# Optimization experiments

Hardware: AMD Instinct MI355X
Metric: run time of the kernel (lower is better)

The kernel has to match this reference:

```python
import jax, jax.numpy as jnp
import numpy as np

NUM_FREQS = 10  # get_embedder_nerf(10, input_dims=3) -> 3 + 3*2*10 = 63 dims


def nerf_embed(x):
    # x: [..., 3]; order per NeRF embedder: [x, sin(f0*x), cos(f0*x), sin(f1*x), ...]
    freqs = (2.0 ** jnp.arange(NUM_FREQS)).astype(x.dtype)           # [10]
    xb = x[..., None, :] * freqs[:, None]                            # [..., 10, 3]
    sc = jnp.stack([jnp.sin(xb), jnp.cos(xb)], axis=-2)              # [..., 10, 2, 3]
    return jnp.concatenate([x, sc.reshape(x.shape[:-1] + (60,))], axis=-1)


def setup_inputs() -> dict:
    key = jax.random.key(0)
    ks = jax.random.split(key, 16)
    B, H, W = 4, 256, 256
    V, F = 50000, 100000
    FEAT, SHAPE_FEAT, STYLE = 256, 128, 256
    D_IN = FEAT + SHAPE_FEAT + 63 + STYLE  # 703
    HID = 256
    s = 0.05
    return {
        "pix_to_face": jax.random.randint(ks[0], (B, H, W), 0, F),
        "bary_coords": jax.random.uniform(ks[1], (B, H, W, 3), dtype=jnp.float32),
        "faces": jax.random.randint(ks[2], (F, 3), 0, V),
        "feature": jax.random.normal(ks[3], (V, FEAT), dtype=jnp.float32),
        "shape_features": jax.random.normal(ks[4], (V, SHAPE_FEAT), dtype=jnp.float32),
        "color_bg": jax.random.uniform(ks[5], (B, 3, 1, 1), dtype=jnp.float32),
        "style_latent": jax.random.normal(ks[6], (1, STYLE), dtype=jnp.float32),
        "w1": jax.random.normal(ks[7], (D_IN, HID), dtype=jnp.float32) * s,
        "b1": jax.random.normal(ks[8], (HID,), dtype=jnp.float32) * s,
        "w2": jax.random.normal(ks[9], (HID, HID), dtype=jnp.float32) * s,
        "b2": jax.random.normal(ks[10], (HID,), dtype=jnp.float32) * s,
        "w3": jax.random.normal(ks[11], (HID, 3), dtype=jnp.float32) * s,
        "b3": jax.random.normal(ks[12], (3,), dtype=jnp.float32) * s,
    }


def reference(pix_to_face, bary_coords, faces, feature, shape_features,
              color_bg, style_latent, w1, b1, w2, b2, w3, b3):
    B, H, W = pix_to_face.shape
    mask = pix_to_face > 0                                           # foreground pixels
    vidx = faces[pix_to_face]                                        # [B,H,W,3] vertex ids
    # gather per-vertex features then barycentric-weighted mean over the 3 verts
    fv = feature[vidx]                                               # [B,H,W,3,256]
    ff = jnp.einsum('bhwvc,bhwv->bhwc', fv, bary_coords) / 3.0       # .mean(dim=3)
    sv = shape_features[vidx]                                        # [B,H,W,3,128]
    sf = jnp.einsum('bhwvc,bhwv->bhwc', sv, bary_coords) / 3.0
    emb = nerf_embed(bary_coords)                                    # [B,H,W,63]
    style = jnp.broadcast_to(style_latent[0], (B, H, W, style_latent.shape[-1]))
    x = jnp.concatenate([ff, sf, emb, style], axis=-1)               # [B,H,W,703]
    h = jax.nn.relu(x @ w1 + b1)
    h = jax.nn.relu(h @ w2 + b2)
    out = jax.nn.relu(h @ w3 + b3)                                   # mlp ends with ReLU
    colors = out - 1.0                                               # use_act=True, tanh=False
    bg = color_bg[:, :, 0, 0][:, None, None, :]                      # [B,1,1,3]
    buf = jnp.where(mask[..., None], colors, bg)                     # scatter to image
    return jnp.concatenate([buf, mask.astype(buf.dtype)[..., None]], axis=-1)  # [B,H,W,4]
```

## Files before the change

### kernel.cpp

```cpp
#include <hip/hip_runtime.h>
#include <math.h>


typedef _Float16 hv8 __attribute__((ext_vector_type(8)));
typedef __attribute__((ext_vector_type(4))) float f32x4;

#define TILE_M 64

__device__ inline int swzE(int row, int k) { return row * 64  + (k ^ ((row & 7) << 3)); }
__device__ inline int swzH(int row, int k) { return row * 256 + (k ^ ((row & 7) << 3)); }
__device__ inline int swzA(int row, int k) { return row * 384 + (k ^ ((row & 7) << 3)); }

__global__ __launch_bounds__(256)
void prep_weights(const float* __restrict__ style,
                  const float* __restrict__ w1, const float* __restrict__ b1,
                  const float* __restrict__ w2, const float* __restrict__ w3,
                  _Float16* __restrict__ w1T, _Float16* __restrict__ w2T,
                  _Float16* __restrict__ w3T, float* __restrict__ b1p)
{
    const int j = blockIdx.x;
    const int t = threadIdx.x;
    if (j < 256) {
        float part = style[t] * w1[(size_t)(447 + t) * 256 + j];
        #pragma unroll
        for (int off = 32; off; off >>= 1) part += __shfl_down(part, off, 64);
        __shared__ float red[4];
        if ((t & 63) == 0) red[t >> 6] = part;
        __syncthreads();
        if (t == 0) b1p[j] = b1[j] + red[0] + red[1] + red[2] + red[3];
        for (int k = t; k < 448; k += 256) {
            float v = (k < 447) ? w1[(size_t)k * 256 + j] : 0.0f;
            if (k < 384) v *= (1.0f / 3.0f);
            w1T[(size_t)j * 448 + k] = (_Float16)v;
        }
    } else if (j < 512) {
        const int jj = j - 256;
        w2T[(size_t)jj * 256 + t] = (_Float16)w2[(size_t)t * 256 + jj];
    } else {
        #pragma unroll
        for (int r = 0; r < 16; ++r)
            w3T[r * 256 + t] = (r < 3) ? (_Float16)w3[t * 3 + r] : (_Float16)0.0f;
    }
}

__global__ __launch_bounds__(256, 2)
void pgemm(const float* __restrict__ feat, const float* __restrict__ shp,
           const _Float16* __restrict__ w1T, _Float16* __restrict__ P, int nV)
{
    __shared__ _Float16 as[64 * 384];
    const int tid = threadIdx.x;
    const int n0 = blockIdx.x * 64;
    const int lane = tid & 63, wv = tid >> 6;
    const int nbase = wv << 6, l15 = lane & 15, kq = lane >> 4;

    const hv8* bp[4];
    #pragma unroll
    for (int nf = 0; nf < 4; ++nf)
        bp[nf] = (const hv8*)(w1T + (size_t)(nbase + nf * 16 + l15) * 448 + (kq << 3));
    hv8 bv[3][4];
    auto loadB = [&](int t, hv8* dst) {
        #pragma unroll
        for (int nf = 0; nf < 4; ++nf) dst[nf] = bp[nf][t << 2];
    };
    loadB(0, bv[0]); loadB(1, bv[1]); loadB(2, bv[2]);

    #pragma unroll
    for (int i = 0; i < 12; ++i) {
        const int id = tid + i * 256;
        const int row = id / 48;
        const int g = id - row * 48;
        int v = n0 + row; if (v >= nV) v = nV - 1;
        const float* s = (g < 32) ? (feat + (size_t)v * 256 + g * 8)
                                  : (shp  + (size_t)v * 128 + (g - 32) * 8);
        const float4 a = ((const float4*)s)[0];
        const float4 b = ((const float4*)s)[1];
        hv8 h = { (_Float16)a.x, (_Float16)a.y, (_Float16)a.z, (_Float16)a.w,
                  (_Float16)b.x, (_Float16)b.y, (_Float16)b.z, (_Float16)b.w };
        *(hv8*)(&as[swzA(row, g * 8)]) = h;
    }
    f32x4 acc[4][4];
    #pragma unroll
    for (int mf = 0; mf < 4; ++mf)
        #pragma unroll
        for (int nf = 0; nf < 4; ++nf) acc[mf][nf] = (f32x4){0.f, 0.f, 0.f, 0.f};
    __syncthreads();

    auto loadA = [&](int t, hv8* dst) {
        #pragma unroll
        for (int mf = 0; mf < 4; ++mf)
            dst[mf] = *(const hv8*)(as + swzA(mf * 16 + l15, (t << 5) | (kq << 3)));
    };
    hv8 av[2][4];
    loadA(0, av[0]);
    #pragma unroll
    for (int t = 0; t < 12; ++t) {
        if (t + 1 < 12) loadA(t + 1, av[(t + 1) & 1]);
        const hv8* avt = av[t & 1];
        const hv8* bvt = bv[t % 3];
        __builtin_amdgcn_s_setprio(1);
        #pragma unroll
        for (int mf = 0; mf < 4; ++mf)
            #pragma unroll
            for (int nf = 0; nf < 4; ++nf)
                acc[mf][nf] = __builtin_amdgcn_mfma_f32_16x16x32_f16(avt[mf], bvt[nf], acc[mf][nf], 0, 0, 0);
        __builtin_amdgcn_s_setprio(0);
        if (t + 3 < 12) loadB(t + 3, bv[t % 3]);
    }
    #pragma unroll
    for (int mf = 0; mf < 4; ++mf)
        #pragma unroll
        for (int nf = 0; nf < 4; ++nf) {
            const int col = nbase + nf * 16 + l15;
            const int r0 = mf * 16 + (kq << 2);
            #pragma unroll
            for (int r = 0; r < 4; ++r) {
                const int v = n0 + r0 + r;
                if (v < nV) P[(size_t)v * 256 + col] = (_Float16)acc[mf][nf][r];
            }
        }
}

__global__ __launch_bounds__(256, 3)
void renderer(const int* __restrict__ pix, const float* __restrict__ bary,
              const int* __restrict__ faces,
              const _Float16* __restrict__ P,
              const float* __restrict__ color_bg,
              const float* __restrict__ b2g,
              const float* __restrict__ b3,
              const _Float16* __restrict__ w1T,
              const _Float16* __restrict__ w2T,
              const _Float16* __restrict__ w3T,
              const float* __restrict__ b1p,
              float* __restrict__ out)
{
    __shared__ _Float16 embs[64 * 64];
    __shared__ _Float16 pb[64 * 256];
    __shared__ int   vidx[TILE_M][3];
    __shared__ float bcs[TILE_M][3];

    const int tid = threadIdx.x;
    const int cpx = gridDim.x >> 3;
    const int bid = (blockIdx.x & 7) * cpx + (blockIdx.x >> 3);
    const int n0  = bid * TILE_M;

    const int lane  = tid & 63;
    const int wv    = tid >> 6;
    const int nbase = wv << 6;
    const int l15   = lane & 15;
    const int kq    = lane >> 4;

    if (tid < TILE_M) {
        const int n = n0 + tid;
        const int face = pix[n];
        vidx[tid][0] = faces[face * 3 + 0];
        vidx[tid][1] = faces[face * 3 + 1];
        vidx[tid][2] = faces[face * 3 + 2];
        bcs[tid][0] = bary[n * 3 + 0];
        bcs[tid][1] = bary[n * 3 + 1];
        bcs[tid][2] = bary[n * 3 + 2];
    }
    __syncthreads();

    const int gp = tid >> 5;
    const int c8 = (tid & 31) << 3;

    hv8 g0[3], g1[3];
    auto loadG = [&](hv8* g, const int b) {
        const int p = b * 8 + gp;
        g[0] = *(const hv8*)(P + (size_t)vidx[p][0] * 256 + c8);
        g[1] = *(const hv8*)(P + (size_t)vidx[p][1] * 256 + c8);
        g[2] = *(const hv8*)(P + (size_t)vidx[p][2] * 256 + c8);
    };
    auto blendG = [&](hv8* g, const int b) {
        const int p = b * 8 + gp;
        const _Float16 c0 = (_Float16)bcs[p][0];
        const _Float16 c1 = (_Float16)bcs[p][1];
        const _Float16 c2 = (_Float16)bcs[p][2];
        *(hv8*)(&pb[swzH(p, c8)]) = g[0] * c0 + g[1] * c1 + g[2] * c2;
    };

    loadG(g0, 0);
    loadG(g1, 1);

    {
        const int p = tid >> 2;
        const int e16 = (tid & 3) << 4;
        const float c0 = bcs[p][0], c1 = bcs[p][1], c2 = bcs[p][2];
        #pragma unroll
        for (int hh = 0; hh < 2; ++hh) {
            hv8 h;
            #pragma unroll
            for (int i = 0; i < 8; ++i) {
                const int s = e16 + hh * 8 + i;
                float v;
                if (s < 3) v = (s == 0) ? c0 : ((s == 1) ? c1 : c2);
                else if (s < 63) {
                    const int q = s - 3;
                    const int f = q / 6;
                    const int rem = q - f * 6;
                    const int d = (rem >= 3) ? rem - 3 : rem;
                    const float bd = (d == 0) ? c0 : ((d == 1) ? c1 : c2);
                    const float arg = bd * (float)(1 << f);
                    v = (rem < 3) ? __sinf(arg) : __cosf(arg);
                } else v = 0.0f;
                h[i] = (_Float16)v;
            }
            *(hv8*)(&embs[swzE(p, e16 + hh * 8)]) = h;
        }
    }

    blendG(g0, 0); loadG(g0, 2);
    blendG(g1, 1); loadG(g1, 3);
    blendG(g0, 2); loadG(g0, 4);
    blendG(g1, 3); loadG(g1, 5);
    blendG(g0, 4); loadG(g0, 6);
    blendG(g1, 5); loadG(g1, 7);
    blendG(g0, 6);
    blendG(g1, 7);

    f32x4 acc[4][4];
    #pragma unroll
    for (int nf = 0; nf < 4; ++nf) {
        const float b = b1p[nbase + nf * 16 + l15];
        #pragma unroll
        for (int mf = 0; mf < 4; ++mf) acc[mf][nf] = (f32x4){b, b, b, b};
    }
    __syncthreads();

    #pragma unroll
    for (int t = 0; t < 2; ++t) {
        hv8 ave[4], bve[4];
        #pragma unroll
        for (int nf = 0; nf < 4; ++nf)
            bve[nf] = *(const hv8*)(w1T + (size_t)(nbase + nf * 16 + l15) * 448 + 384 + (t << 5) + (kq << 3));
        #pragma unroll
        for (int mf = 0; mf < 4; ++mf)
            ave[mf] = *(const hv8*)(embs + swzE(mf * 16 + l15, (t << 5) | (kq << 3)));
        __builtin_amdgcn_s_setprio(1);
        #pragma unroll
        for (int mf = 0; mf < 4; ++mf)
            #pragma unroll
            for (int nf = 0; nf < 4; ++nf)
                acc[mf][nf] = __builtin_amdgcn_mfma_f32_16x16x32_f16(ave[mf], bve[nf], acc[mf][nf], 0, 0, 0);
        __builtin_amdgcn_s_setprio(0);
    }

    #pragma unroll
    for (int mf = 0; mf < 4; ++mf)
        #pragma unroll
        for (int nf = 0; nf < 4; ++nf) {
            const int col = nbase + nf * 16 + l15;
            const int r0 = mf * 16 + (kq << 2);
            #pragma unroll
            for (int r = 0; r < 4; ++r) {
                const int sl = swzH(r0 + r, col);
                const float pv = (float)pb[sl];
                pb[sl] = (_Float16)fmaxf(acc[mf][nf][r] + pv, 0.0f);
            }
            const float b = b2g[col];
            acc[mf][nf] = (f32x4){b, b, b, b};
        }
    __syncthreads();

    const hv8* bp2[4];
    #pragma unroll
    for (int nf = 0; nf < 4; ++nf)
        bp2[nf] = (const hv8*)(w2T + (size_t)(nbase + nf * 16 + l15) * 256 + (kq << 3));
    #pragma unroll
    for (int t = 0; t < 8; ++t) {
        hv8 av[4], bv[4];
        #pragma unroll
        for (int nf = 0; nf < 4; ++nf) bv[nf] = bp2[nf][t << 2];
        #pragma unroll
        for (int mf = 0; mf < 4; ++mf)
            av[mf] = *(const hv8*)(pb + swzH(mf * 16 + l15, (t << 5) | (kq << 3)));
        __builtin_amdgcn_s_setprio(1);
        #pragma unroll
        for (int mf = 0; mf < 4; ++mf)
            #pragma unroll
            for (int nf = 0; nf < 4; ++nf)
                acc[mf][nf] = __builtin_amdgcn_mfma_f32_16x16x32_f16(av[mf], bv[nf], acc[mf][nf], 0, 0, 0);
        __builtin_amdgcn_s_setprio(0);
    }

    __syncthreads();
    #pragma unroll
    for (int mf = 0; mf < 4; ++mf)
        #pragma unroll
        for (int nf = 0; nf < 4; ++nf) {
            const int col = nbase + nf * 16 + l15;
            const int r0 = mf * 16 + (kq << 2);
            #pragma unroll
            for (int r = 0; r < 4; ++r)
                pb[swzH(r0 + r, col)] = (_Float16)fmaxf(acc[mf][nf][r], 0.0f);
        }

    hv8 bw3[8];
    #pragma unroll
    for (int t = 0; t < 8; ++t)
        bw3[t] = *(const hv8*)(w3T + l15 * 256 + ((t << 5) | (kq << 3)));
    __syncthreads();

    f32x4 acc3 = (f32x4){0.f, 0.f, 0.f, 0.f};
    #pragma unroll
    for (int t = 0; t < 8; ++t) {
        const hv8 av3 = *(const hv8*)(pb + swzH((wv << 4) + l15, (t << 5) | (kq << 3)));
        acc3 = __builtin_amdgcn_mfma_f32_16x16x32_f16(av3, bw3[t], acc3, 0, 0, 0);
    }
    if (l15 < 4) {
        const int ch = l15;
        #pragma unroll
        for (int r = 0; r < 4; ++r) {
            const int p = (wv << 4) + (kq << 2) + r;
            const int n = n0 + p;
            const bool m = pix[n] > 0;
            float v;
            if (ch == 3) v = m ? 1.0f : 0.0f;
            else         v = m ? (fmaxf(acc3[r] + b3[ch], 0.0f) - 1.0f)
                               : color_bg[(n >> 16) * 3 + ch];
            out[(size_t)n * 4 + ch] = v;
        }
    }
}

extern "C" void kernel_launch(void* const* d_in, const int* in_sizes, int n_in,
                              void* d_out, int out_size, void* d_ws, size_t ws_size,
                              hipStream_t stream) {
    const int*   pix      = (const int*)  d_in[0];
    const float* bary     = (const float*)d_in[1];
    const int*   faces    = (const int*)  d_in[2];
    const float* feature  = (const float*)d_in[3];
    const float* shapef   = (const float*)d_in[4];
    const float* color_bg = (const float*)d_in[5];
    const float* style    = (const float*)d_in[6];
    const float* w1       = (const float*)d_in[7];
    const float* b1       = (const float*)d_in[8];
    const float* w2       = (const float*)d_in[9];
    const float* b2       = (const float*)d_in[10];
    const float* w3       = (const float*)d_in[11];
    const float* b3       = (const float*)d_in[12];
    float* out = (float*)d_out;

    const int nV = in_sizes[3] / 256;

    char* ws = (char*)d_ws;
    _Float16* w1T  = (_Float16*)ws;
    _Float16* w2T  = (_Float16*)(ws + 229376);
    float*    b1p  = (float*)   (ws + 360448);
    _Float16* w3T  = (_Float16*)(ws + 361472);
    _Float16* Ptab = (_Float16*)(ws + 369664);

    hipLaunchKernelGGL(prep_weights, dim3(513), dim3(256), 0, stream,
                       style, w1, b1, w2, w3, w1T, w2T, w3T, b1p);
    hipLaunchKernelGGL(pgemm, dim3((nV + 63) / 64), dim3(256), 0, stream,
                       feature, shapef, w1T, Ptab, nV);

    const int npix = in_sizes[0];
    hipLaunchKernelGGL(renderer, dim3(npix / TILE_M), dim3(256), 0, stream,
                       pix, bary, faces, Ptab, color_bg,
                       b2, b3, w1T, w2T, w3T, b1p, out);
}
```

Baseline: 185.7 us.

## Make each wave own 16 pixel rows end to end and drop block barriers

The renderer now gives each wave its own 16-pixel slice and private shared buffer, running gather, blend, all three MLP layers and output without __syncthreads, using only lgkmcnt waits. The embedding fragment is built directly in registers, and the b1 bias is folded into the blended gathered features. Shared memory per block shrinks and launch bounds rise to 4 blocks per SM to raise occupancy. In exchange, each wave now reads all of w1/w2 from global/L1 per 16 rows instead of sharing a 64-row tile, so weight traffic per pixel grows roughly fourfold, and b1 is now added in fp16 rather than fp32.

```diff
diff --git a/kernel.cpp b/kernel.cpp
--- a/kernel.cpp
+++ b/kernel.cpp
@@ -7,8 +7,7 @@
 
 #define TILE_M 64
 
-__device__ inline int swzE(int row, int k) { return row * 64  + (k ^ ((row & 7) << 3)); }
-__device__ inline int swzH(int row, int k) { return row * 256 + (k ^ ((row & 7) << 3)); }
+__device__ inline int swzW(int row, int k) { return row * 256 + (k ^ ((row & 7) << 3)); }
 __device__ inline int swzA(int row, int k) { return row * 384 + (k ^ ((row & 7) << 3)); }
 
 __global__ __launch_bounds__(256)
@@ -120,78 +119,70 @@
         }
 }
 
-__global__ __launch_bounds__(256, 3)
+__global__ __launch_bounds__(256, 4)
 void renderer(const int* __restrict__ pix, const float* __restrict__ bary,
               const int* __restrict__ faces,
               const _Float16* __restrict__ P,
               const float* __restrict__ color_bg,
               const float* __restrict__ b2g,
-              const float* __restrict__ b3,
+              const float* __restrict__ b3g,
               const _Float16* __restrict__ w1T,
               const _Float16* __restrict__ w2T,
               const _Float16* __restrict__ w3T,
               const float* __restrict__ b1p,
               float* __restrict__ out)
 {
-    __shared__ _Float16 embs[64 * 64];
-    __shared__ _Float16 pb[64 * 256];
-    __shared__ int   vidx[TILE_M][3];
-    __shared__ float bcs[TILE_M][3];
-
-    const int tid = threadIdx.x;
-    const int cpx = gridDim.x >> 3;
-    const int bid = (blockIdx.x & 7) * cpx + (blockIdx.x >> 3);
-    const int n0  = bid * TILE_M;
-
-    const int lane  = tid & 63;
-    const int wv    = tid >> 6;
-    const int nbase = wv << 6;
-    const int l15   = lane & 15;
-    const int kq    = lane >> 4;
-
-    if (tid < TILE_M) {
-        const int n = n0 + tid;
+    __shared__ _Float16 pbAll[4][16 * 256];
+    __shared__ int   vidx[4][16][3];
+    __shared__ float bcs[4][16][3];
+
+    const int tid  = threadIdx.x;
+    const int lane = tid & 63;
+    const int wv   = tid >> 6;
+    const int cpx  = gridDim.x >> 3;
+    const int bid  = (blockIdx.x & 7) * cpx + (blockIdx.x >> 3);
+    const int n0   = bid * TILE_M + wv * 16;
+    const int l15  = lane & 15;
+    const int kq   = lane >> 4;
+    _Float16* pbw = &pbAll[wv][0];
+
+    if (lane < 16) {
+        const int n = n0 + lane;
         const int face = pix[n];
-        vidx[tid][0] = faces[face * 3 + 0];
-        vidx[tid][1] = faces[face * 3 + 1];
-        vidx[tid][2] = faces[face * 3 + 2];
-        bcs[tid][0] = bary[n * 3 + 0];
-        bcs[tid][1] = bary[n * 3 + 1];
-        bcs[tid][2] = bary[n * 3 + 2];
-    }
-    __syncthreads();
-
-    const int gp = tid >> 5;
-    const int c8 = (tid & 31) << 3;
-
+        vidx[wv][lane][0] = faces[face * 3 + 0];
+        vidx[wv][lane][1] = faces[face * 3 + 1];
+        vidx[wv][lane][2] = faces[face * 3 + 2];
+        bcs[wv][lane][0] = bary[n * 3 + 0];
+        bcs[wv][lane][1] = bary[n * 3 + 1];
+        bcs[wv][lane][2] = bary[n * 3 + 2];
+    }
+    asm volatile("s_waitcnt lgkmcnt(0)" ::: "memory");
+
+    const int gp = lane >> 5;
+    const int c8 = (lane & 31) << 3;
     hv8 g0[3], g1[3];
-    auto loadG = [&](hv8* g, const int b) {
-        const int p = b * 8 + gp;
-        g[0] = *(const hv8*)(P + (size_t)vidx[p][0] * 256 + c8);
-        g[1] = *(const hv8*)(P + (size_t)vidx[p][1] * 256 + c8);
-        g[2] = *(const hv8*)(P + (size_t)vidx[p][2] * 256 + c8);
+    auto loadG = [&](hv8* g, int b) {
+        const int p = (b << 1) + gp;
+        g[0] = *(const hv8*)(P + (size_t)vidx[wv][p][0] * 256 + c8);
+        g[1] = *(const hv8*)(P + (size_t)vidx[wv][p][1] * 256 + c8);
+        g[2] = *(const hv8*)(P + (size_t)vidx[wv][p][2] * 256 + c8);
     };
-    auto blendG = [&](hv8* g, const int b) {
-        const int p = b * 8 + gp;
-        const _Float16 c0 = (_Float16)bcs[p][0];
-        const _Float16 c1 = (_Float16)bcs[p][1];
-        const _Float16 c2 = (_Float16)bcs[p][2];
-        *(hv8*)(&pb[swzH(p, c8)]) = g[0] * c0 + g[1] * c1 + g[2] * c2;
-    };
-
     loadG(g0, 0);
     loadG(g1, 1);
 
+    const float4 bb0 = *(const float4*)(b1p + c8);
+    const float4 bb1 = *(const float4*)(b1p + c8 + 4);
+    const hv8 b1h = { (_Float16)bb0.x, (_Float16)bb0.y, (_Float16)bb0.z, (_Float16)bb0.w,
+                      (_Float16)bb1.x, (_Float16)bb1.y, (_Float16)bb1.z, (_Float16)bb1.w };
+
+    hv8 ave[2];
     {
-        const int p = tid >> 2;
-        const int e16 = (tid & 3) << 4;
-        const float c0 = bcs[p][0], c1 = bcs[p][1], c2 = bcs[p][2];
-        #pragma unroll
-        for (int hh = 0; hh < 2; ++hh) {
-            hv8 h;
+        const float c0 = bcs[wv][l15][0], c1 = bcs[wv][l15][1], c2 = bcs[wv][l15][2];
+        #pragma unroll
+        for (int t = 0; t < 2; ++t) {
             #pragma unroll
             for (int i = 0; i < 8; ++i) {
-                const int s = e16 + hh * 8 + i;
+                const int s = (t << 5) + (kq << 3) + i;
                 float v;
                 if (s < 3) v = (s == 0) ? c0 : ((s == 1) ? c1 : c2);
                 else if (s < 63) {
@@ -203,12 +194,18 @@
                     const float arg = bd * (float)(1 << f);
                     v = (rem < 3) ? __sinf(arg) : __cosf(arg);
                 } else v = 0.0f;
-                h[i] = (_Float16)v;
+                ave[t][i] = (_Float16)v;
             }
-            *(hv8*)(&embs[swzE(p, e16 + hh * 8)]) = h;
-        }
-    }
-
+        }
+    }
+
+    auto blendG = [&](hv8* g, int b) {
+        const int p = (b << 1) + gp;
+        const _Float16 d0 = (_Float16)bcs[wv][p][0];
+        const _Float16 d1 = (_Float16)bcs[wv][p][1];
+        const _Float16 d2 = (_Float16)bcs[wv][p][2];
+        *(hv8*)(&pbw[swzW(p, c8)]) = g[0] * d0 + g[1] * d1 + g[2] * d2 + b1h;
+    };
     blendG(g0, 0); loadG(g0, 2);
     blendG(g1, 1); loadG(g1, 3);
     blendG(g0, 2); loadG(g0, 4);
@@ -217,106 +214,92 @@
     blendG(g1, 5); loadG(g1, 7);
     blendG(g0, 6);
     blendG(g1, 7);
-
-    f32x4 acc[4][4];
-    #pragma unroll
-    for (int nf = 0; nf < 4; ++nf) {
-        const float b = b1p[nbase + nf * 16 + l15];
-        #pragma unroll
-        for (int mf = 0; mf < 4; ++mf) acc[mf][nf] = (f32x4){b, b, b, b};
-    }
-    __syncthreads();
-
-    #pragma unroll
-    for (int t = 0; t < 2; ++t) {
-        hv8 ave[4], bve[4];
-        #pragma unroll
-        for (int nf = 0; nf < 4; ++nf)
-            bve[nf] = *(const hv8*)(w1T + (size_t)(nbase + nf * 16 + l15) * 448 + 384 + (t << 5) + (kq << 3));
-        #pragma unroll
-        for (int mf = 0; mf < 4; ++mf)
-            ave[mf] = *(const hv8*)(embs + swzE(mf * 16 + l15, (t << 5) | (kq << 3)));
-        __builtin_amdgcn_s_setprio(1);
-        #pragma unroll
-        for (int mf = 0; mf < 4; ++mf)
-            #pragma unroll
-            for (int nf = 0; nf < 4; ++nf)
-                acc[mf][nf] = __builtin_amdgcn_mfma_f32_16x16x32_f16(ave[mf], bve[nf], acc[mf][nf], 0, 0, 0);
-        __builtin_amdgcn_s_setprio(0);
-    }
-
-    #pragma unroll
-    for (int mf = 0; mf < 4; ++mf)
-        #pragma unroll
-        for (int nf = 0; nf < 4; ++nf) {
-            const int col = nbase + nf * 16 + l15;
-            const int r0 = mf * 16 + (kq << 2);
-            #pragma unroll
-            for (int r = 0; r < 4; ++r) {
-                const int sl = swzH(r0 + r, col);
-                const float pv = (float)pb[sl];
-                pb[sl] = (_Float16)fmaxf(acc[mf][nf][r] + pv, 0.0f);
+    asm volatile("s_waitcnt lgkmcnt(0)" ::: "memory");
+
+    #pragma unroll
+    for (int h = 0; h < 2; ++h) {
+        const int cb = h << 7;
+        f32x4 acc[8];
+        #pragma unroll
+        for (int n = 0; n < 8; ++n) {
+            const int col = cb + n * 16 + l15;
+            const int r0 = kq << 2;
+            #pragma unroll
+            for (int r = 0; r < 4; ++r)
+                acc[n][r] = (float)pbw[swzW(r0 + r, col)];
+        }
+        #pragma unroll
+        for (int t = 0; t < 2; ++t) {
+            __builtin_amdgcn_s_setprio(1);
+            #pragma unroll
+            for (int n = 0; n < 8; ++n) {
+                const hv8 bve = *(const hv8*)(w1T + (size_t)(cb + n * 16 + l15) * 448 + 384 + (t << 5) + (kq << 3));
+                acc[n] = __builtin_amdgcn_mfma_f32_16x16x32_f16(ave[t], bve, acc[n], 0, 0, 0);
             }
-            const float b = b2g[col];
-            acc[mf][nf] = (f32x4){b, b, b, b};
-        }
-    __syncthreads();
-
-    const hv8* bp2[4];
-    #pragma unroll
-    for (int nf = 0; nf < 4; ++nf)
-        bp2[nf] = (const hv8*)(w2T + (size_t)(nbase + nf * 16 + l15) * 256 + (kq << 3));
+            __builtin_amdgcn_s_setprio(0);
+        }
+        #pragma unroll
+        for (int n = 0; n < 8; ++n) {
+            const int col = cb + n * 16 + l15;
+            const int r0 = kq << 2;
+            #pragma unroll
+            for (int r = 0; r < 4; ++r)
+                pbw[swzW(r0 + r, col)] = (_Float16)fmaxf(acc[n][r], 0.0f);
+        }
+    }
+    asm volatile("s_waitcnt lgkmcnt(0)" ::: "memory");
+
+    hv8 avh[8];
+    #pragma unroll
+    for (int t = 0; t < 8; ++t)
+        avh[t] = *(const hv8*)(pbw + swzW(l15, (t << 5) | (kq << 3)));
+    #pragma unroll
+    for (int h = 0; h < 2; ++h) {
+        const int cb = h << 7;
+        f32x4 acc[8];
+        #pragma unroll
+        for (int n = 0; n < 8; ++n) {
+            const float b = b2g[cb + n * 16 + l15];
+            acc[n] = (f32x4){b, b, b, b};
+        }
+        #pragma unroll
+        for (int t = 0; t < 8; ++t) {
+            __builtin_amdgcn_s_setprio(1);
+            #pragma unroll
+            for (int n = 0; n < 8; ++n) {
+                const hv8 bv = *(const hv8*)(w2T + (size_t)(cb + n * 16 + l15) * 256 + (t << 5) + (kq << 3));
+                acc[n] = __builtin_amdgcn_mfma_f32_16x16x32_f16(avh[t], bv, acc[n], 0, 0, 0);
+            }
+            __builtin_amdgcn_s_setprio(0);
+        }
+        #pragma unroll
+        for (int n = 0; n < 8; ++n) {
+            const int col = cb + n * 16 + l15;
+            const int r0 = kq << 2;
+            #pragma unroll
+            for (int r = 0; r < 4; ++r)
+                pbw[swzW(r0 + r, col)] = (_Float16)fmaxf(acc[n][r], 0.0f);
+        }
+    }
+    asm volatile("s_waitcnt lgkmcnt(0)" ::: "memory");
+
+    f32x4 acc3 = (f32x4){0.f, 0.f, 0.f, 0.f};
     #pragma unroll
     for (int t = 0; t < 8; ++t) {
-        hv8 av[4], bv[4];
-        #pragma unroll
-        for (int nf = 0; nf < 4; ++nf) bv[nf] = bp2[nf][t << 2];
-        #pragma unroll
-        for (int mf = 0; mf < 4; ++mf)
-            av[mf] = *(const hv8*)(pb + swzH(mf * 16 + l15, (t << 5) | (kq << 3)));
-        __builtin_amdgcn_s_setprio(1);
-        #pragma unroll
-        for (int mf = 0; mf < 4; ++mf)
-            #pragma unroll
-            for (int nf = 0; nf < 4; ++nf)
-                acc[mf][nf] = __builtin_amdgcn_mfma_f32_16x16x32_f16(av[mf], bv[nf], acc[mf][nf], 0, 0, 0);
-        __builtin_amdgcn_s_setprio(0);
-    }
-
-    __syncthreads();
-    #pragma unroll
-    for (int mf = 0; mf < 4; ++mf)
-        #pragma unroll
-        for (int nf = 0; nf < 4; ++nf) {
-            const int col = nbase + nf * 16 + l15;
-            const int r0 = mf * 16 + (kq << 2);
-            #pragma unroll
-            for (int r = 0; r < 4; ++r)
-                pb[swzH(r0 + r, col)] = (_Float16)fmaxf(acc[mf][nf][r], 0.0f);
-        }
-
-    hv8 bw3[8];
-    #pragma unroll
-    for (int t = 0; t < 8; ++t)
-        bw3[t] = *(const hv8*)(w3T + l15 * 256 + ((t << 5) | (kq << 3)));
-    __syncthreads();
-
-    f32x4 acc3 = (f32x4){0.f, 0.f, 0.f, 0.f};
-    #pragma unroll
-    for (int t = 0; t < 8; ++t) {
-        const hv8 av3 = *(const hv8*)(pb + swzH((wv << 4) + l15, (t << 5) | (kq << 3)));
-        acc3 = __builtin_amdgcn_mfma_f32_16x16x32_f16(av3, bw3[t], acc3, 0, 0, 0);
+        const hv8 a3 = *(const hv8*)(pbw + swzW(l15, (t << 5) | (kq << 3)));
+        const hv8 b3v = *(const hv8*)(w3T + l15 * 256 + (t << 5) + (kq << 3));
+        acc3 = __builtin_amdgcn_mfma_f32_16x16x32_f16(a3, b3v, acc3, 0, 0, 0);
     }
     if (l15 < 4) {
         const int ch = l15;
         #pragma unroll
         for (int r = 0; r < 4; ++r) {
-            const int p = (wv << 4) + (kq << 2) + r;
+            const int p = (kq << 2) + r;
             const int n = n0 + p;
             const bool m = pix[n] > 0;
             float v;
             if (ch == 3) v = m ? 1.0f : 0.0f;
-            else         v = m ? (fmaxf(acc3[r] + b3[ch], 0.0f) - 1.0f)
+            else         v = m ? (fmaxf(acc3[r] + b3g[ch], 0.0f) - 1.0f)
                                : color_bg[(n >> 16) * 3 + ch];
             out[(size_t)n * 4 + ch] = v;
         }
```

Result: slower. 418.3 us (+125.2%).
